# Kernel tuning notes

Hardware: AMD Instinct MI355X
Metric: run time of the kernel (lower is better)

## Reference

```python
import jax, jax.numpy as jnp
import numpy as np

B, T, D, H, A = 1024, 128, 64, 256, 8  # batch, seq_len, state_dim, hidden_dim, action_dim


def setup_inputs() -> dict:
    key = jax.random.key(0)
    ks = jax.random.split(key, 12)
    k = 1.0 / np.sqrt(H)  # PyTorch LSTM/Linear default init range
    u = lambda kk, shape: jax.random.uniform(kk, shape, jnp.float32, -k, k)
    return {
        "state": jax.random.normal(ks[0], (B, 1, D), jnp.float32),
        "gamma": jnp.ones((D,), jnp.float32),
        "beta": jnp.zeros((D,), jnp.float32),
        "W_ih0": u(ks[1], (4 * H, D)),
        "W_hh0": u(ks[2], (4 * H, H)),
        "b_ih0": u(ks[3], (4 * H,)),
        "b_hh0": u(ks[4], (4 * H,)),
        "W_ih1": u(ks[5], (4 * H, H)),
        "W_hh1": u(ks[6], (4 * H, H)),
        "b_ih1": u(ks[7], (4 * H,)),
        "b_hh1": u(ks[8], (4 * H,)),
        "fcW": u(ks[9], (A, H)),
        "fcb": u(ks[10], (A,)),
        "seq_len": T,
    }


def _lstm_cell(x, h, c, Wih, Whh, b):
    # PyTorch gate order: input, forget, cell(g), output
    g = x @ Wih.T + h @ Whh.T + b
    i, f, gg, o = jnp.split(g, 4, axis=-1)
    c_new = jax.nn.sigmoid(f) * c + jax.nn.sigmoid(i) * jnp.tanh(gg)
    h_new = jax.nn.sigmoid(o) * jnp.tanh(c_new)
    return h_new, c_new


def reference(state, gamma, beta, W_ih0, W_hh0, b_ih0, b_hh0,
              W_ih1, W_hh1, b_ih1, b_hh1, fcW, fcb, seq_len):
    # state: [B, 1, D]; the same (layernormed) input is fed every timestep,
    # only the LSTM hidden/cell state evolves.
    x = state[:, 0, :]  # [B, D]
    mu = x.mean(-1, keepdims=True)
    var = ((x - mu) ** 2).mean(-1, keepdims=True)
    xn = (x - mu) * jax.lax.rsqrt(var + 1e-5) * gamma + beta  # LayerNorm(state_dim)

    b0 = b_ih0 + b_hh0
    b1 = b_ih1 + b_hh1
    bsz = x.shape[0]
    hdim = W_hh0.shape[1]
    z = jnp.zeros((bsz, hdim), x.dtype)
    init = (z, z, z, z)  # (h0, c0, h1, c1); h=None -> zeros in torch

    def step(carry, _):
        h0, c0, h1, c1 = carry
        h0, c0 = _lstm_cell(xn, h0, c0, W_ih0, W_hh0, b0)  # layer 0
        h1, c1 = _lstm_cell(h0, h1, c1, W_ih1, W_hh1, b1)  # layer 1
        action = jnp.tanh(h1 @ fcW.T + fcb)  # [B, A]
        return (h0, c0, h1, c1), action

    _, actions = jax.lax.scan(step, init, None, length=seq_len)  # [T, B, A]
    return jnp.transpose(actions, (1, 0, 2))  # [B, T, A]
```

## Files before the change

kernel.cpp:

```cpp
#include <hip/hip_runtime.h>
#include <math.h>

#define B_    1024
#define T_    128
#define D_    64
#define H_    256
#define A_    8

#define NG    8
#define NB    32
#define MB    128
#define SL    8
#define FSTR  32

typedef __attribute__((ext_vector_type(8))) short short8;
typedef __attribute__((ext_vector_type(4))) float floatx4;

__device__ __forceinline__ short f2bf(float f) {
    union { float f; unsigned u; } x; x.f = f;
    return (short)((x.u + 0x7FFFu + ((x.u >> 16) & 1u)) >> 16);
}
__device__ __forceinline__ float bf2f(short s) {
    union { unsigned u; float f; } x;
    x.u = ((unsigned)(unsigned short)s) << 16;
    return x.f;
}
__device__ __forceinline__ float sigm(float x) {
    return __builtin_amdgcn_rcpf(1.0f + __expf(-x));
}
__device__ __forceinline__ float ftanh(float x) {
    float t = __expf(-2.0f * fabsf(x));
    float r = (1.0f - t) * __builtin_amdgcn_rcpf(1.0f + t);
    return copysignf(r, x);
}

__device__ __forceinline__ void cell_update(floatx4 aA, floatx4 aB, float* cpair,
                                            short* __restrict__ Hw, size_t rowbase,
                                            int colbase, int hi, int rsel) {
    floatx4 tA, tB;
#pragma unroll
    for (int r = 0; r < 4; ++r) {
        tA[r] = __shfl_xor(aA[r], 8, 64);
        tB[r] = __shfl_xor(aB[r], 8, 64);
    }
#pragma unroll
    for (int rr = 0; rr < 2; ++rr) {
        int r = rsel + rr;
        float gi = hi ? tA[r] : aA[r];
        float gf = hi ? aA[r] : tA[r];
        float gg = hi ? tB[r] : aB[r];
        float go = hi ? aB[r] : tB[r];
        float cn = sigm(gf) * cpair[rr] + sigm(gi) * ftanh(gg);
        float hn = sigm(go) * ftanh(cn);
        cpair[rr] = cn;
        Hw[(rowbase + r) * H_ + colbase] = f2bf(hn);
    }
}

__global__ void __launch_bounds__(512, 2)
actor_kernel(const float* __restrict__ state, const float* __restrict__ gamma,
             const float* __restrict__ beta,  const float* __restrict__ Wih0,
             const float* __restrict__ Whh0,  const float* __restrict__ bih0,
             const float* __restrict__ bhh0,  const float* __restrict__ Wih1,
             const float* __restrict__ Whh1,  const float* __restrict__ bih1,
             const float* __restrict__ bhh1,  const float* __restrict__ fcW,
             const float* __restrict__ fcb,   float* __restrict__ out,
             unsigned* __restrict__ flags, unsigned* __restrict__ xccArr,
             short* __restrict__ Hb0, short* __restrict__ Hb1)
{
    __shared__ __attribute__((aligned(16))) short sWp[24576];

    const int blk  = blockIdx.x;
    const int g    = blk & 7;
    const int s    = blk >> 3;
    const int tid  = threadIdx.x;
    const int lane = tid & 63;
    const int wave = tid >> 6;
    const int g128 = g * MB;

    const int q4   = lane >> 4;
    const int l15  = lane & 15;
    const int jj   = l15 & 7;
    const int hi   = l15 >> 3;
    const int rg0  = hi * H_ + s * SL + jj;
    const int rg1  = (2 + hi) * H_ + s * SL + jj;
    const int mrow = wave * 16 + q4 * 4;
    const int colbase = s * SL + jj;
    const int rsel = hi * 2;

    unsigned xcc;
    asm volatile("s_getreg_b32 %0, hwreg(HW_REG_XCC_ID)" : "=s"(xcc));
    if (tid == 0) xccArr[blk] = xcc + 1u;

    float* sXn = (float*)sWp;
    if (tid < MB) {
        const float* xr = state + (size_t)(g128 + tid) * D_;
        float mu = 0.f;
        for (int d = 0; d < D_; ++d) mu += xr[d];
        mu *= (1.0f / D_);
        float var = 0.f;
        for (int d = 0; d < D_; ++d) { float t = xr[d] - mu; var += t * t; }
        var *= (1.0f / D_);
        float is = rsqrtf(var + 1e-5f);
        for (int d = 0; d < D_; ++d)
            sXn[tid * 65 + d] = (xr[d] - mu) * is * gamma[d] + beta[d];
    }
    __syncthreads();

    const float b0v0 = bih0[rg0] + bhh0[rg0];
    const float b0v1 = bih0[rg1] + bhh0[rg1];
    const float b1v0 = bih1[rg0] + bhh1[rg0];
    const float b1v1 = bih1[rg1] + bhh1[rg1];

    floatx4 pre0a, pre0b;
    {
        const float* w0 = Wih0 + (size_t)rg0 * D_;
        const float* w1 = Wih0 + (size_t)rg1 * D_;
#pragma unroll
        for (int r = 0; r < 4; ++r) { pre0a[r] = b0v0; pre0b[r] = b0v1; }
        for (int d = 0; d < D_; ++d) {
            float wa = w0[d], wb = w1[d];
#pragma unroll
            for (int r = 0; r < 4; ++r) {
                float xv = sXn[(mrow + r) * 65 + d];
                pre0a[r] += xv * wa;
                pre0b[r] += xv * wb;
            }
        }
    }
    __syncthreads();

    const int fo = lane >> 3, fk8 = lane & 7;
    float fcw_r[32];
#pragma unroll
    for (int kk = 0; kk < 32; ++kk) fcw_r[kk] = fcW[fo * H_ + fk8 * 32 + kk];
    const float fcb_r = fcb[fo];

    for (int idx = tid; idx < 8192; idx += 512) {
        int kt = idx >> 10, rem = idx & 1023;
        int c = rem >> 9, rem2 = rem & 511;
        int ln = rem2 >> 3, j = rem2 & 7;
        int q4_ = ln >> 4, l15_ = ln & 15;
        int n = c * 16 + l15_;
        int r = (n >> 3) * H_ + s * SL + (n & 7);
        int k = kt * 32 + q4_ * 8 + j;
        sWp[idx] = f2bf(Whh0[(size_t)r * H_ + k]);
    }
    for (int idx = tid; idx < 16384; idx += 512) {
        int kt = idx >> 11, rem = idx & 2047;
        int c = rem >> 9, rem2 = rem & 511;
        int ln = rem2 >> 3, j = rem2 & 7;
        int q4_ = ln >> 4, l15_ = ln & 15;
        int n = (c & 1) * 16 + l15_;
        int r = (n >> 3) * H_ + s * SL + (n & 7);
        int k = kt * 32 + q4_ * 8 + j;
        float v = (c >> 1) ? Whh1[(size_t)r * H_ + k] : Wih1[(size_t)r * H_ + k];
        sWp[8192 + idx] = f2bf(v);
    }
    float c0[2] = {0.f, 0.f}, c1[2] = {0.f, 0.f};

    __syncthreads();
    if (tid == 0) {
        __builtin_amdgcn_fence(__ATOMIC_RELEASE, "agent");
        __hip_atomic_store(&flags[(g * NB + s) * FSTR], 1u,
                           __ATOMIC_RELAXED, __HIP_MEMORY_SCOPE_AGENT);
    }
    if (wave == 7 && lane < NB) {
        while (__hip_atomic_load(&flags[(g * NB + lane) * FSTR],
                                 __ATOMIC_RELAXED, __HIP_MEMORY_SCOPE_AGENT) < 1u)
            __builtin_amdgcn_s_sleep(1);
    }
    __syncthreads();
    __builtin_amdgcn_fence(__ATOMIC_ACQUIRE, "agent");
    bool fastp = true;
    {
        unsigned x0 = xccArr[g];
        for (int j2 = 1; j2 < NB; ++j2)
            fastp = fastp && (xccArr[g + 8 * j2] == x0);
    }

    const short* ldsB = sWp + lane * 8;

    const int BH = B_ * H_;
    for (int ph = 0; ph <= T_ + 1; ++ph) {
        const short* H0r  = Hb0 + ((ph + 1) & 1) * BH;
        short*       H0w  = Hb0 + (ph & 1) * BH;
        const short* H1r2 = Hb1 + (ph & 1) * BH;
        short*       H1w  = Hb1 + ((ph + 1) & 1) * BH;

        const bool doL0 = (ph < T_);
        const bool doL1 = (ph >= 1 && ph <= T_);

        if (doL0 || doL1) {
            short8 a0[8], a1[8];
            const short* ap = H0r + (size_t)(g128 + wave * 16 + l15) * H_ + q4 * 8;
#pragma unroll
            for (int kt = 0; kt < 8; ++kt)
                a0[kt] = *(const short8*)(ap + kt * 32);
            if (doL1) {
                const short* cp = H1r2 + (size_t)(g128 + wave * 16 + l15) * H_ + q4 * 8;
#pragma unroll
                for (int kt = 0; kt < 8; ++kt)
                    a1[kt] = *(const short8*)(cp + kt * 32);
            }

            floatx4 l0a = pre0a, l0b = pre0b, l1a, l1b;
#pragma unroll
            for (int r = 0; r < 4; ++r) { l1a[r] = b1v0; l1b[r] = b1v1; }

#pragma unroll
            for (int kt = 0; kt < 8; ++kt) {
                if (doL0) {
                    short8 b0a = *(const short8*)(ldsB + kt * 1024);
                    short8 b0b = *(const short8*)(ldsB + kt * 1024 + 512);
                    l0a = __builtin_amdgcn_mfma_f32_16x16x32_bf16(a0[kt], b0a, l0a, 0, 0, 0);
                    l0b = __builtin_amdgcn_mfma_f32_16x16x32_bf16(a0[kt], b0b, l0b, 0, 0, 0);
                }
                if (doL1) {
                    short8 bia = *(const short8*)(ldsB + 8192 + kt * 2048);
                    short8 bib = *(const short8*)(ldsB + 8192 + kt * 2048 + 512);
                    short8 bha = *(const short8*)(ldsB + 8192 + kt * 2048 + 1024);
                    short8 bhb = *(const short8*)(ldsB + 8192 + kt * 2048 + 1536);
                    l1a = __builtin_amdgcn_mfma_f32_16x16x32_bf16(a0[kt], bia, l1a, 0, 0, 0);
                    l1b = __builtin_amdgcn_mfma_f32_16x16x32_bf16(a0[kt], bib, l1b, 0, 0, 0);
                    l1a = __builtin_amdgcn_mfma_f32_16x16x32_bf16(a1[kt], bha, l1a, 0, 0, 0);
                    l1b = __builtin_amdgcn_mfma_f32_16x16x32_bf16(a1[kt], bhb, l1b, 0, 0, 0);
                }
            }

            size_t rowbase = (size_t)(g128 + mrow);
            if (doL0) cell_update(l0a, l0b, c0, H0w, rowbase, colbase, hi, rsel);
            if (doL1) cell_update(l1a, l1b, c1, H1w, rowbase, colbase, hi, rsel);
        }

        if (ph <= T_) {
            __syncthreads();
            if (tid == 0) {
                if (!fastp) __builtin_amdgcn_fence(__ATOMIC_RELEASE, "agent");
                __hip_atomic_store(&flags[(g * NB + s) * FSTR], (unsigned)(ph + 2),
                                   __ATOMIC_RELAXED, __HIP_MEMORY_SCOPE_AGENT);
            }
            if (ph >= 2 && wave < 4) {
                int t = ph - 2;
                int b = 4 * s + wave;
                const short8* hp = (const short8*)(H1r2 + (size_t)(g128 + b) * H_ + fk8 * 32);
                float sum = 0.f;
#pragma unroll
                for (int c8 = 0; c8 < 4; ++c8) {
                    short8 hv = hp[c8];
#pragma unroll
                    for (int j = 0; j < 8; ++j)
                        sum += bf2f(hv[j]) * fcw_r[c8 * 8 + j];
                }
                sum += __shfl_down(sum, 4, 8);
                sum += __shfl_down(sum, 2, 8);
                sum += __shfl_down(sum, 1, 8);
                if (fk8 == 0)
                    out[((size_t)(g128 + b) * T_ + t) * A_ + fo] = ftanh(sum + fcb_r);
            }
            if (wave == 7 && lane < NB) {
                while (__hip_atomic_load(&flags[(g * NB + lane) * FSTR],
                                         __ATOMIC_RELAXED, __HIP_MEMORY_SCOPE_AGENT)
                       < (unsigned)(ph + 2)) {  }
            }
            __syncthreads();
            if (fastp) { asm volatile("buffer_inv sc0" ::: "memory"); }
            else       { __builtin_amdgcn_fence(__ATOMIC_ACQUIRE, "agent"); }
        } else if (wave < 4) {
            int t = ph - 2;
            int b = 4 * s + wave;
            const short8* hp = (const short8*)(H1r2 + (size_t)(g128 + b) * H_ + fk8 * 32);
            float sum = 0.f;
#pragma unroll
            for (int c8 = 0; c8 < 4; ++c8) {
                short8 hv = hp[c8];
#pragma unroll
                for (int j = 0; j < 8; ++j)
                    sum += bf2f(hv[j]) * fcw_r[c8 * 8 + j];
            }
            sum += __shfl_down(sum, 4, 8);
            sum += __shfl_down(sum, 2, 8);
            sum += __shfl_down(sum, 1, 8);
            if (fk8 == 0)
                out[((size_t)(g128 + b) * T_ + t) * A_ + fo] = ftanh(sum + fcb_r);
        }
    }
}

extern "C" void kernel_launch(void* const* d_in, const int* in_sizes, int n_in,
                              void* d_out, int out_size, void* d_ws, size_t ws_size,
                              hipStream_t stream)
{
    const float* state = (const float*)d_in[0];
    const float* gamma = (const float*)d_in[1];
    const float* beta  = (const float*)d_in[2];
    const float* Wih0  = (const float*)d_in[3];
    const float* Whh0  = (const float*)d_in[4];
    const float* bih0  = (const float*)d_in[5];
    const float* bhh0  = (const float*)d_in[6];
    const float* Wih1  = (const float*)d_in[7];
    const float* Whh1  = (const float*)d_in[8];
    const float* bih1  = (const float*)d_in[9];
    const float* bhh1  = (const float*)d_in[10];
    const float* fcW   = (const float*)d_in[11];
    const float* fcb   = (const float*)d_in[12];
    float* out = (float*)d_out;

    unsigned* flags  = (unsigned*)d_ws;
    unsigned* xccArr = (unsigned*)((char*)d_ws + 32768);
    short* Hb0 = (short*)((char*)d_ws + 36864);
    short* Hb1 = Hb0 + 2 * B_ * H_;

    size_t zbytes = 36864 + (size_t)4 * B_ * H_ * sizeof(short);
    hipMemsetAsync(d_ws, 0, zbytes, stream);

    void* args[] = { &state, &gamma, &beta, &Wih0, &Whh0, &bih0, &bhh0,
                     &Wih1, &Whh1, &bih1, &bhh1, &fcW, &fcb, &out,
                     &flags, &xccArr, &Hb0, &Hb1 };
    hipError_t err = hipLaunchCooperativeKernel((const void*)actor_kernel,
                                                dim3(NG * NB), dim3(512),
                                                args, 0, stream);
    if (err != hipSuccess) {
        (void)hipGetLastError();
        actor_kernel<<<dim3(NG * NB), dim3(512), 0, stream>>>(
            state, gamma, beta, Wih0, Whh0, bih0, bhh0,
            Wih1, Whh1, bih1, bhh1, fcW, fcb, out, flags, xccArr, Hb0, Hb1);
    }
    (void)in_sizes; (void)n_in; (void)out_size; (void)ws_size;
}
```

Before: 968.3 us.

## Remap blocks to groups by XCC so each group sits on one die

Each block now reads its XCC id and takes a slot with a per-XCC atomic counter. After a grid-wide arrival barrier it derives its group and slice so that all 32 blocks of a batch group land on the same XCC. This lets the cheap buffer_inv sc0 path be used instead of agent-scope acquire fences, and keeps per-step flag traffic within one die's L2; it falls back to the static mapping when the XCC counts are not multiples of 32. The per-step spin-wait also gains s_sleep to cut polling pressure, which may add some wake-up latency.

New measurement: 966.2 us. About the same (-0.2%).

```diff
diff --git a/kernel.cpp b/kernel.cpp
--- a/kernel.cpp
+++ b/kernel.cpp
@@ -65,18 +65,46 @@
              const float* __restrict__ Whh1,  const float* __restrict__ bih1,
              const float* __restrict__ bhh1,  const float* __restrict__ fcW,
              const float* __restrict__ fcb,   float* __restrict__ out,
-             unsigned* __restrict__ flags, unsigned* __restrict__ xccArr,
+             unsigned* __restrict__ flags, unsigned* __restrict__ aux,
              short* __restrict__ Hb0, short* __restrict__ Hb1)
 {
     __shared__ __attribute__((aligned(16))) short sWp[24576];
+    __shared__ int sMap[3];
 
     const int blk  = blockIdx.x;
-    const int g    = blk & 7;
-    const int s    = blk >> 3;
     const int tid  = threadIdx.x;
     const int lane = tid & 63;
     const int wave = tid >> 6;
-    const int g128 = g * MB;
+
+    if (tid == 0) {
+        unsigned xcc;
+        asm volatile("s_getreg_b32 %0, hwreg(HW_REG_XCC_ID)" : "=s"(xcc));
+        xcc &= 7u;
+        unsigned r = atomicAdd(&aux[xcc * 16], 1u);
+        __hip_atomic_fetch_add(&aux[256], 1u, __ATOMIC_ACQ_REL,
+                               __HIP_MEMORY_SCOPE_AGENT);
+        while (__hip_atomic_load(&aux[256], __ATOMIC_RELAXED,
+                                 __HIP_MEMORY_SCOPE_AGENT) < (unsigned)gridDim.x)
+            __builtin_amdgcn_s_sleep(1);
+        __builtin_amdgcn_fence(__ATOMIC_ACQUIRE, "agent");
+        int pre = 0, tot = 0; bool ok = true;
+        for (int x = 0; x < 8; ++x) {
+            int cx = (int)__hip_atomic_load(&aux[x * 16], __ATOMIC_RELAXED,
+                                            __HIP_MEMORY_SCOPE_AGENT);
+            if (cx & 31) ok = false;
+            if (x < (int)xcc) pre += cx >> 5;
+            tot += cx >> 5;
+        }
+        if (tot != NG) ok = false;
+        sMap[0] = ok ? (pre + (int)(r >> 5)) : (blk & 7);
+        sMap[1] = ok ? (int)(r & 31)         : (blk >> 3);
+        sMap[2] = ok ? 1 : 0;
+    }
+    __syncthreads();
+    const int  g     = sMap[0];
+    const int  s     = sMap[1];
+    const bool fastp = (sMap[2] != 0);
+    const int  g128  = g * MB;
 
     const int q4   = lane >> 4;
     const int l15  = lane & 15;
@@ -87,10 +115,6 @@
     const int mrow = wave * 16 + q4 * 4;
     const int colbase = s * SL + jj;
     const int rsel = hi * 2;
-
-    unsigned xcc;
-    asm volatile("s_getreg_b32 %0, hwreg(HW_REG_XCC_ID)" : "=s"(xcc));
-    if (tid == 0) xccArr[blk] = xcc + 1u;
 
     float* sXn = (float*)sWp;
     if (tid < MB) {
@@ -158,26 +182,7 @@
         sWp[8192 + idx] = f2bf(v);
     }
     float c0[2] = {0.f, 0.f}, c1[2] = {0.f, 0.f};
-
     __syncthreads();
-    if (tid == 0) {
-        __builtin_amdgcn_fence(__ATOMIC_RELEASE, "agent");
-        __hip_atomic_store(&flags[(g * NB + s) * FSTR], 1u,
-                           __ATOMIC_RELAXED, __HIP_MEMORY_SCOPE_AGENT);
-    }
-    if (wave == 7 && lane < NB) {
-        while (__hip_atomic_load(&flags[(g * NB + lane) * FSTR],
-                                 __ATOMIC_RELAXED, __HIP_MEMORY_SCOPE_AGENT) < 1u)
-            __builtin_amdgcn_s_sleep(1);
-    }
-    __syncthreads();
-    __builtin_amdgcn_fence(__ATOMIC_ACQUIRE, "agent");
-    bool fastp = true;
-    {
-        unsigned x0 = xccArr[g];
-        for (int j2 = 1; j2 < NB; ++j2)
-            fastp = fastp && (xccArr[g + 8 * j2] == x0);
-    }
 
     const short* ldsB = sWp + lane * 8;
 
@@ -261,7 +266,8 @@
             if (wave == 7 && lane < NB) {
                 while (__hip_atomic_load(&flags[(g * NB + lane) * FSTR],
                                          __ATOMIC_RELAXED, __HIP_MEMORY_SCOPE_AGENT)
-                       < (unsigned)(ph + 2)) {  }
+                       < (unsigned)(ph + 2))
+                    __builtin_amdgcn_s_sleep(1);
             }
             __syncthreads();
             if (fastp) { asm volatile("buffer_inv sc0" ::: "memory"); }
@@ -306,8 +312,8 @@
     const float* fcb   = (const float*)d_in[12];
     float* out = (float*)d_out;
 
-    unsigned* flags  = (unsigned*)d_ws;
-    unsigned* xccArr = (unsigned*)((char*)d_ws + 32768);
+    unsigned* flags = (unsigned*)d_ws;
+    unsigned* aux   = (unsigned*)((char*)d_ws + 32768);
     short* Hb0 = (short*)((char*)d_ws + 36864);
     short* Hb1 = Hb0 + 2 * B_ * H_;
 
@@ -316,7 +322,7 @@
 
     void* args[] = { &state, &gamma, &beta, &Wih0, &Whh0, &bih0, &bhh0,
                      &Wih1, &Whh1, &bih1, &bhh1, &fcW, &fcb, &out,
-                     &flags, &xccArr, &Hb0, &Hb1 };
+                     &flags, &aux, &Hb0, &Hb1 };
     hipError_t err = hipLaunchCooperativeKernel((const void*)actor_kernel,
                                                 dim3(NG * NB), dim3(512),
                                                 args, 0, stream);
@@ -324,7 +330,7 @@
         (void)hipGetLastError();
         actor_kernel<<<dim3(NG * NB), dim3(512), 0, stream>>>(
             state, gamma, beta, Wih0, Whh0, bih0, bhh0,
-            Wih1, Whh1, bih1, bhh1, fcW, fcb, out, flags, xccArr, Hb0, Hb1);
+            Wih1, Whh1, bih1, bhh1, fcW, fcb, out, flags, aux, Hb0, Hb1);
     }
     (void)in_sizes; (void)n_in; (void)out_size; (void)ws_size;
 }
```
